# Optimization experiments

Measured on AMD Instinct MI355X. Metric: run time of the kernel, lower is better.

Reference implementation:

```python
import jax, jax.numpy as jnp
import numpy as np

N, R, E, H, F = 50000, 6, 32768, 256, 16
NH, HD = 8, 32
EPS_LN = 1e-5

def _ln(x, g, b):
    mu = x.mean(-1, keepdims=True)
    var = ((x - mu) ** 2).mean(-1, keepdims=True)
    return (x - mu) * jax.lax.rsqrt(var + EPS_LN) * g + b

def setup_inputs() -> dict:
    key = jax.random.key(0)
    ks = jax.random.split(key, 32)
    s = lambda i, shape, scale=0.05: jax.random.normal(ks[i], shape, jnp.float32) * scale
    return {
        'x': jax.random.normal(ks[0], (N, H), jnp.float32),
        'edge_index': jax.random.randint(ks[1], (R, 2, E), 0, N, jnp.int32),
        'edge_attr': jax.random.normal(ks[2], (R, E, F), jnp.float32),
        'Wq': s(3, (R, H, H)), 'bq': s(4, (R, H)),
        'Wk': s(5, (R, H + F, H)), 'bk': s(6, (R, H)),
        'Wv': s(7, (R, H + F, H)), 'bv': s(8, (R, H)),
        'prior': jnp.ones((R, NH), jnp.float32),
        'Wm': s(9, (R, H, H)), 'bm': s(10, (R, H)),
        'W_ir1': s(11, (R * H, H)), 'b_ir1': s(12, (H,)),
        'W_ir2': s(13, (H, R)), 'b_ir2': s(14, (R,)),
        'Wmp': s(15, (3, H, H)), 'bmp': s(16, (3, H)),
        'Wa1': s(17, (H, H // 2)), 'ba1': s(18, (H // 2,)),
        'Wa2': s(19, (H // 2, 1)),
        'g_meta': jnp.ones((H,), jnp.float32), 'b_meta': jnp.zeros((H,), jnp.float32),
        'Wc': s(20, (2 * H, H)), 'bc': s(21, (H,)),
        'g_out': jnp.ones((H,), jnp.float32), 'b_out': jnp.zeros((H,), jnp.float32),
    }

def _block(x, edge_index, edge_attr, Wq, bq, Wk, bk, Wv, bv, prior, Wm, bm,
           W_ir1, b_ir1, W_ir2, b_ir2, Wmp, bmp, Wa1, ba1, Wa2, g_meta, b_meta,
           Wc, bc, g_out, b_out):
    def rel_layer(eidx, eattr, wq, bq_, wk, bk_, wv, bv_, pr, wm, bm_):
        src, dst = eidx[0], eidx[1]
        q = x @ wq + bq_                                  # [N,H]
        kv_in = jnp.concatenate([x[src], eattr], -1)      # [E,H+F]
        k = (kv_in @ wk + bk_).reshape(E, NH, HD)
        v = (kv_in @ wv + bv_).reshape(E, NH, HD)
        qe = q[dst].reshape(E, NH, HD)
        scores = (qe * k).sum(-1) / np.sqrt(HD) * pr      # [E,NH]
        m = jax.ops.segment_max(scores, dst, num_segments=N)
        ex = jnp.exp(scores - m[dst])
        denom = jax.ops.segment_sum(ex, dst, num_segments=N)
        w = ex / (denom[dst] + 1e-16)
        wv_flat = (w[..., None] * v).reshape(E, H)
        agg = jax.ops.segment_sum(wv_flat, dst, num_segments=N)  # [N,H]
        return jax.nn.gelu(agg @ wm + bm_, approximate=False)

    rel_out = jax.vmap(rel_layer)(edge_index, edge_attr, Wq, bq, Wk, bk, Wv, bv,
                                  prior, Wm, bm)          # [R,N,H]

    all_rel = jnp.transpose(rel_out, (1, 0, 2)).reshape(N, R * H)
    h = jax.nn.gelu(all_rel @ W_ir1 + b_ir1, approximate=False)
    inter_w = jax.nn.softmax(h @ W_ir2 + b_ir2, axis=-1)  # [N,R]
    inter_agg = jnp.einsum('nr,rnh->nh', inter_w, rel_out)

    # meta-paths: 0=entangle(ENTANGLE=2,SWAP=3) 1=control(CONTROL=4,ROTATION=0) 2=local(PAULI=1,TEMPORAL=5)
    paths = jnp.stack([rel_out[2] + rel_out[3], rel_out[4] + rel_out[0],
                       rel_out[1] + rel_out[5]], axis=1)  # [N,3,H]
    stacked = jnp.einsum('nph,phk->npk', paths, Wmp) + bmp
    attn = jax.nn.softmax((jnp.tanh(stacked @ Wa1 + ba1) @ Wa2).squeeze(-1), axis=1)
    meta = _ln((attn[..., None] * stacked).sum(1), g_meta, b_meta)

    combined = jax.nn.gelu(jnp.concatenate([inter_agg, meta], -1) @ Wc + bc,
                           approximate=False)
    return _ln(x + combined, g_out, b_out)

def reference(x, edge_index, edge_attr, Wq, bq, Wk, bk, Wv, bv, prior, Wm, bm,
              W_ir1, b_ir1, W_ir2, b_ir2, Wmp, bmp, Wa1, ba1, Wa2, g_meta, b_meta,
              Wc, bc, g_out, b_out):
    return _block(x, edge_index, edge_attr, Wq, bq, Wk, bk, Wv, bv, prior, Wm, bm,
                  W_ir1, b_ir1, W_ir2, b_ir2, Wmp, bmp, Wa1, ba1, Wa2,
                  g_meta, b_meta, Wc, bc, g_out, b_out)
```

## Files before the change

### kernel.cpp

```cpp
#include <hip/hip_runtime.h>
#include <hip/hip_bf16.h>

typedef __hip_bfloat16 bf16;
typedef __attribute__((ext_vector_type(8))) short short8;
typedef __attribute__((ext_vector_type(4))) float f32x4;

#define NN 50000
#define RR 6
#define EE 32768
#define HH 256
#define FF 16
#define NHEAD 8
#define KVP 320

struct __align__(8) bf16x4 { bf16 v[4]; };

__device__ __forceinline__ float b2f(bf16 v) { return __bfloat162float(v); }
__device__ __forceinline__ bf16 f2b(float v) { return __float2bfloat16(v); }
__device__ __forceinline__ short f2s(float f) { bf16 b = f2b(f); return __builtin_bit_cast(short, b); }
__device__ __forceinline__ float s2f(short s) { return b2f(__builtin_bit_cast(bf16, s)); }
__device__ __forceinline__ float gelu_f(float x) { return 0.5f * x * (1.0f + erff(x * 0.7071067811865476f)); }

__device__ __forceinline__ void gl2lds16(const void* g, void* l) {
  __builtin_amdgcn_global_load_lds(
      (const __attribute__((address_space(1))) unsigned int*)g,
      (__attribute__((address_space(3))) unsigned int*)l, 16, 0, 0);
}

__global__ void zero_k(uint4* __restrict__ p, int n16)
{
  const uint4 z = make_uint4(0u, 0u, 0u, 0u);
  for (int i = blockIdx.x * blockDim.x + threadIdx.x; i < n16; i += gridDim.x * blockDim.x)
    p[i] = z;
}

__global__ void cvt_k(const float* __restrict__ in, bf16* __restrict__ out, int n4)
{
  const int i = blockIdx.x * 256 + threadIdx.x;
  if (i >= n4) return;
  const float4 f = ((const float4*)in)[i];
  bf16x4 o; o.v[0] = f2b(f.x); o.v[1] = f2b(f.y); o.v[2] = f2b(f.z); o.v[3] = f2b(f.w);
  ((bf16x4*)out)[i] = o;
}

__global__ void tconv_k(const float* __restrict__ in, bf16* __restrict__ out,
                        int K, int NC, int Kp, long izs, long ozs)
{
  __shared__ float t[32][33];
  in  += (size_t)blockIdx.z * izs;
  out += (size_t)blockIdx.z * ozs;
  const int kb = blockIdx.x * 32, nb = blockIdx.y * 32;
  const int tx = threadIdx.x & 31, ty = threadIdx.x >> 5;
  for (int i = ty; i < 32; i += 8) {
    const int k = kb + i, n = nb + tx;
    t[i][tx] = (k < K && n < NC) ? in[(size_t)k * NC + n] : 0.f;
  }
  __syncthreads();
  for (int i = ty; i < 32; i += 8) {
    const int n = nb + i, k = kb + tx;
    if (n < NC && k < Kp) out[(size_t)n * Kp + k] = f2b(t[tx][i]);
  }
}

__global__ void bkv_k(const float* __restrict__ bk, const float* __restrict__ bv,
                      float* __restrict__ bkv)
{
  const int i = blockIdx.x * 256 + threadIdx.x;
  if (i >= RR * 512) return;
  const int r = i >> 9, c = i & 511;
  bkv[i] = (c < 256) ? bk[r * 256 + c] : bv[r * 256 + (c - 256)];
}

__global__ void copyslot_k(const bf16* __restrict__ tmp, bf16* __restrict__ slot)
{
  const int i = blockIdx.x * 256 + threadIdx.x;
  if (i >= NN * 32) return;
  const int n = i >> 5, c = (i & 31) * 8;
  *(short8*)(slot + (size_t)n * 1536 + c) = *(const short8*)(tmp + (size_t)n * 256 + c);
}

template<int ASRC, int ACT, int ZMODE, typename TO>
__global__ __launch_bounds__(256) void mm_k(
    const void* __restrict__ Av, const bf16* __restrict__ A2, int lda,
    const int* __restrict__ src, const bf16* __restrict__ eab,
    const float* __restrict__ dnm,
    const bf16* __restrict__ Bt, const float* __restrict__ bias,
    const float* __restrict__ wa2, TO* __restrict__ C, int ldc,
    float* __restrict__ logits, int M, int K, int z0)
{
  __shared__ short lds[2 * 128 * 64];
  const int tid = threadIdx.x;
  const int w = tid >> 6, l = tid & 63;
  const int col0 = blockIdx.x << 7;
  const int row0 = blockIdx.y << 7;
  const bf16* Ab = (const bf16*)Av;
  const bf16* A2b = A2;
  const bf16* Btz = Bt;
  const float* biasz = bias;
  TO* Cz = C;
  float* lg = logits;
  const int* srcz = src;
  const int* dstz = nullptr;
  const bf16* eabz = eab;
  const bf16* qz = nullptr;
  float* exbz = nullptr;
  float* dnmaz = nullptr;
  const float* priz = nullptr;
  if constexpr (ZMODE == 1) {
    const int slots3[3] = {2, 4, 1};
    Ab = (const bf16*)Av + slots3[blockIdx.z] * 256;
    lg = logits + (size_t)blockIdx.z * M;
  } else if constexpr (ZMODE == 3) {
    const int r1s[3] = {2, 4, 1}, r2s[3] = {3, 0, 5};
    const int z = blockIdx.z + z0;
    Ab  = (const bf16*)Av + (size_t)r1s[z] * 256;
    A2b = A2 + (size_t)r2s[z] * 256;
    Btz = Bt + (size_t)z * 256 * K;
    biasz = bias + z * 256;
    Cz = C + (size_t)blockIdx.z * (size_t)M * 256;
  } else if constexpr (ZMODE == 4) {
    const int z = blockIdx.z;
    srcz  = src + (size_t)z * 2 * EE;
    dstz  = srcz + EE;
    eabz  = eab + (size_t)z * EE * FF;
    qz    = A2 + z * 256;
    Btz   = Bt + (size_t)z * 512 * KVP;
    biasz = bias + z * 512;
    Cz    = C + (size_t)z * (size_t)EE * 256;
    exbz  = logits + (size_t)z * EE * NHEAD;
    dnmaz = logits + (size_t)2 * EE * NHEAD + (size_t)z * NN * NHEAD;
    priz  = dnm + z * NHEAD;
  }
  const int wm = (w >> 1) << 6, wn = (w & 1) << 6;
  const int lane15 = l & 15, kq = l >> 4;

  f32x4 acc[4][4] = {};

  for (int k0 = 0; k0 < K; k0 += 64) {
#pragma unroll
    for (int i = 0; i < 4; ++i) {
      const int idx = (w * 4 + i) * 64 + l;
      const int row = idx >> 3, cg = idx & 7;
      const int scg = cg ^ (row & 7);
      const int r = min(row0 + row, M - 1);
      const int kc = k0 + scg * 8;
      if constexpr (ASRC == 0) {
        gl2lds16(Ab + (size_t)r * lda + kc, &lds[idx * 8]);
      } else if constexpr (ASRC == 2) {
        const short8 u  = *(const short8*)(Ab  + (size_t)r * lda + kc);
        const short8 v2 = *(const short8*)(A2b + (size_t)r * lda + kc);
        short8 s;
#pragma unroll
        for (int j = 0; j < 8; ++j) s[j] = f2s(s2f(u[j]) + s2f(v2[j]));
        *(short8*)&lds[idx * 8] = s;
      } else if constexpr (ASRC == 3) {
        short8 s;
        if (kc < HH) {
          s = *(const short8*)((const bf16*)Av + (size_t)srcz[r] * HH + kc);
        } else if (kc < HH + FF) {
          s = *(const short8*)(eabz + (size_t)r * FF + (kc - HH));
        } else {
#pragma unroll
          for (int j = 0; j < 8; ++j) s[j] = 0;
        }
        *(short8*)&lds[idx * 8] = s;
      } else {
        const float* p = (const float*)Av + (size_t)r * lda + kc;
        const float4 f0 = *(const float4*)p;
        const float4 f1 = *(const float4*)(p + 4);
        const float iv = 1.0f / (dnm[r * NHEAD + (kc >> 5)] + 1e-16f);
        short8 s;
        s[0] = f2s(f0.x * iv); s[1] = f2s(f0.y * iv); s[2] = f2s(f0.z * iv); s[3] = f2s(f0.w * iv);
        s[4] = f2s(f1.x * iv); s[5] = f2s(f1.y * iv); s[6] = f2s(f1.z * iv); s[7] = f2s(f1.w * iv);
        *(short8*)&lds[idx * 8] = s;
      }
    }
#pragma unroll
    for (int i = 0; i < 4; ++i) {
      const int idx = (w * 4 + i) * 64 + l;
      const int row = idx >> 3, cg = idx & 7;
      const int scg = cg ^ (row & 7);
      gl2lds16(Btz + (size_t)(col0 + row) * K + k0 + scg * 8, &lds[8192 + idx * 8]);
    }
    __syncthreads();
#pragma unroll
    for (int kk = 0; kk < 64; kk += 32) {
      short8 af[4], bfr[4];
#pragma unroll
      for (int t = 0; t < 4; ++t) {
        const int ra = wm + t * 16 + lane15;
        const int ca = ((kk >> 3) + kq) ^ (ra & 7);
        af[t] = *(const short8*)&lds[ra * 64 + ca * 8];
        const int rb = wn + t * 16 + lane15;
        const int cb = ((kk >> 3) + kq) ^ (rb & 7);
        bfr[t] = *(const short8*)&lds[8192 + rb * 64 + cb * 8];
      }
#pragma unroll
      for (int ti = 0; ti < 4; ++ti)
#pragma unroll
        for (int tj = 0; tj < 4; ++tj)
          acc[ti][tj] = __builtin_amdgcn_mfma_f32_16x16x32_bf16(af[ti], bfr[tj], acc[ti][tj], 0, 0, 0);
    }
    __syncthreads();
  }

  if constexpr (ZMODE == 4) {
    if (blockIdx.x < 2) {
#pragma unroll
      for (int i = 0; i < 8; ++i) {
        const int idx = (w * 8 + i) * 64 + l;
        const int row = idx >> 4, cg = idx & 15;
        const int d = dstz[row0 + row];
        gl2lds16(qz + (size_t)d * 1536 + col0 + cg * 8, &lds[idx * 8]);
      }
      __syncthreads();
      const int hb = (col0 + wn) >> 5;
      const float pr0 = priz[hb], pr1 = priz[hb + 1];
#pragma unroll
      for (int ti = 0; ti < 4; ++ti) {
#pragma unroll
        for (int reg = 0; reg < 4; ++reg) {
          const int row = wm + ti * 16 + kq * 4 + reg;
          float p0 = 0.f, p1 = 0.f;
#pragma unroll
          for (int tj = 0; tj < 4; ++tj) {
            const int colL = wn + tj * 16 + lane15;
            const float kv_ = acc[ti][tj][reg] + biasz[col0 + colL];
            const float qv = s2f(lds[(row << 7) + colL]);
            if (tj < 2) p0 += qv * kv_; else p1 += qv * kv_;
          }
#pragma unroll
          for (int off = 1; off < 16; off <<= 1) {
            p0 += __shfl_xor(p0, off, 64);
            p1 += __shfl_xor(p1, off, 64);
          }
          if (lane15 == 0) {
            const int e = row0 + row;
            const int d = dstz[e];
            const float e0 = expf(p0 * 0.1767766952966369f * pr0);
            const float e1 = expf(p1 * 0.1767766952966369f * pr1);
            exbz[e * NHEAD + hb]     = e0;
            exbz[e * NHEAD + hb + 1] = e1;
            atomicAdd(&dnmaz[d * NHEAD + hb],     e0);
            atomicAdd(&dnmaz[d * NHEAD + hb + 1], e1);
          }
        }
      }
    } else {
#pragma unroll
      for (int ti = 0; ti < 4; ++ti) {
#pragma unroll
        for (int reg = 0; reg < 4; ++reg) {
          const int row = row0 + wm + ti * 16 + kq * 4 + reg;
#pragma unroll
          for (int tj = 0; tj < 4; ++tj) {
            const int col = col0 + wn + tj * 16 + lane15;
            const float v = acc[ti][tj][reg] + biasz[col];
            Cz[(size_t)row * 256 + (col - 256)] = (TO)f2b(v);
          }
        }
      }
    }
  } else if constexpr (ZMODE != 1) {
#pragma unroll
    for (int ti = 0; ti < 4; ++ti) {
#pragma unroll
      for (int reg = 0; reg < 4; ++reg) {
        const int row = row0 + wm + ti * 16 + kq * 4 + reg;
        if (row >= M) continue;
#pragma unroll
        for (int tj = 0; tj < 4; ++tj) {
          const int col = col0 + wn + tj * 16 + lane15;
          float v = acc[ti][tj][reg] + biasz[col];
          if constexpr (ACT == 1) v = gelu_f(v);
          if constexpr (sizeof(TO) == 2) Cz[(size_t)row * ldc + col] = (TO)f2b(v);
          else                           Cz[(size_t)row * ldc + col] = (TO)v;
        }
      }
    }
  } else {
#pragma unroll
    for (int ti = 0; ti < 4; ++ti) {
#pragma unroll
      for (int reg = 0; reg < 4; ++reg) {
        float part = 0.f;
#pragma unroll
        for (int tj = 0; tj < 4; ++tj) {
          const int col = col0 + wn + tj * 16 + lane15;
          part += tanhf(acc[ti][tj][reg] + biasz[col]) * wa2[col];
        }
#pragma unroll
        for (int off = 8; off > 0; off >>= 1) part += __shfl_xor(part, off, 64);
        const int row = row0 + wm + ti * 16 + kq * 4 + reg;
        if (lane15 == 0 && row < M) atomicAdd(&lg[row], part);
      }
    }
  }
}

__global__ void edge2_k(const float* __restrict__ ex, const bf16* __restrict__ v,
                        const int* __restrict__ dst_idx, float* __restrict__ agg)
{
  const int e = blockIdx.x, t = threadIdx.x;
  const int dst = dst_idx[e];
  const float w = ex[e * NHEAD + (t >> 5)];
  atomicAdd(&agg[(size_t)dst * HH + t], w * b2f(v[(size_t)e * HH + t]));
}

__global__ void interw_k(const bf16* __restrict__ h, const float* __restrict__ W2,
                         const float* __restrict__ b2, float* __restrict__ interw)
{
  const int wv = threadIdx.x >> 6, ln = threadIdx.x & 63;
  const int n = blockIdx.x * 4 + wv;
  if (n >= NN) return;
  float a[6] = {0.f, 0.f, 0.f, 0.f, 0.f, 0.f};
#pragma unroll
  for (int kq = 0; kq < 4; ++kq) {
    const int k = ln + (kq << 6);
    const float hv = b2f(h[(size_t)n * HH + k]);
#pragma unroll
    for (int j = 0; j < 6; ++j) a[j] += hv * W2[k * 6 + j];
  }
#pragma unroll
  for (int j = 0; j < 6; ++j) {
#pragma unroll
    for (int off = 32; off > 0; off >>= 1) a[j] += __shfl_down(a[j], off, 64);
  }
  if (ln == 0) {
    float lg[6], e[6], mx = -1e30f, s = 0.f;
#pragma unroll
    for (int j = 0; j < 6; ++j) { lg[j] = a[j] + b2[j]; mx = fmaxf(mx, lg[j]); }
#pragma unroll
    for (int j = 0; j < 6; ++j) { e[j] = expf(lg[j] - mx); s += e[j]; }
    const float inv = 1.0f / s;
#pragma unroll
    for (int j = 0; j < 6; ++j) interw[(size_t)n * 6 + j] = e[j] * inv;
  }
}

__global__ void interagg_k(const float* __restrict__ interw, const bf16* __restrict__ rel_cat,
                           bf16* __restrict__ comb)
{
  const int n = blockIdx.x, t = threadIdx.x;
  float acc = 0.f;
#pragma unroll
  for (int r = 0; r < 6; ++r)
    acc += interw[(size_t)n * 6 + r] * b2f(rel_cat[(size_t)n * 1536 + r * 256 + t]);
  comb[(size_t)n * 512 + t] = f2b(acc);
}

__global__ void metafinal_k(const float* __restrict__ logits, const bf16* __restrict__ rel_cat,
                            const float* __restrict__ gmeta, const float* __restrict__ bmeta,
                            bf16* __restrict__ comb)
{
  const int wv = threadIdx.x >> 6, ln = threadIdx.x & 63;
  const int n = blockIdx.x * 4 + wv;
  if (n >= NN) return;
  const float l0 = logits[n], l1 = logits[NN + n], l2 = logits[2 * NN + n];
  const float mx = fmaxf(l0, fmaxf(l1, l2));
  const float e0 = expf(l0 - mx), e1 = expf(l1 - mx), e2 = expf(l2 - mx);
  const float inv = 1.0f / (e0 + e1 + e2);
  const float a0 = e0 * inv, a1 = e1 * inv, a2 = e2 * inv;
  const size_t base = (size_t)n * 1536;
  float pre[4], s = 0.f, s2 = 0.f;
#pragma unroll
  for (int q4 = 0; q4 < 4; ++q4) {
    const int j = ln + (q4 << 6);
    const float v = a0 * b2f(rel_cat[base + 2 * 256 + j])
                  + a1 * b2f(rel_cat[base + 4 * 256 + j])
                  + a2 * b2f(rel_cat[base + 1 * 256 + j]);
    pre[q4] = v; s += v; s2 += v * v;
  }
#pragma unroll
  for (int off = 32; off > 0; off >>= 1) { s += __shfl_down(s, off, 64); s2 += __shfl_down(s2, off, 64); }
  s = __shfl(s, 0, 64); s2 = __shfl(s2, 0, 64);
  const float mu = s * (1.0f / 256.0f);
  const float var = s2 * (1.0f / 256.0f) - mu * mu;
  const float rs = rsqrtf(var + 1e-5f);
#pragma unroll
  for (int q4 = 0; q4 < 4; ++q4) {
    const int j = ln + (q4 << 6);
    comb[(size_t)n * 512 + 256 + j] = f2b((pre[q4] - mu) * rs * gmeta[j] + bmeta[j]);
  }
}

__global__ void final_k(const float* __restrict__ x, const float* __restrict__ combined,
                        const float* __restrict__ g, const float* __restrict__ b,
                        float* __restrict__ out)
{
  __shared__ float sred[8];
  const int n = blockIdx.x, t = threadIdx.x;
  const float v = x[(size_t)n * HH + t] + combined[(size_t)n * HH + t];
  float s = v, s2 = v * v;
#pragma unroll
  for (int off = 32; off > 0; off >>= 1) { s += __shfl_down(s, off, 64); s2 += __shfl_down(s2, off, 64); }
  const int wv = t >> 6;
  if ((t & 63) == 0) { sred[wv] = s; sred[4 + wv] = s2; }
  __syncthreads();
  const float st = sred[0] + sred[1] + sred[2] + sred[3];
  const float st2 = sred[4] + sred[5] + sred[6] + sred[7];
  const float mu = st * (1.0f / 256.0f);
  const float var = st2 * (1.0f / 256.0f) - mu * mu;
  const float rs = rsqrtf(var + 1e-5f);
  out[(size_t)n * HH + t] = (v - mu) * rs * g[t] + b[t];
}

extern "C" void kernel_launch(void* const* d_in, const int* in_sizes, int n_in,
                              void* d_out, int out_size, void* d_ws, size_t ws_size,
                              hipStream_t stream)
{
  const float* x      = (const float*)d_in[0];
  const int*   eidx   = (const int*)d_in[1];
  const float* eattr  = (const float*)d_in[2];
  const float* Wq     = (const float*)d_in[3];
  const float* bq     = (const float*)d_in[4];
  const float* Wk     = (const float*)d_in[5];
  const float* bk     = (const float*)d_in[6];
  const float* Wv     = (const float*)d_in[7];
  const float* bv     = (const float*)d_in[8];
  const float* prior  = (const float*)d_in[9];
  const float* Wm     = (const float*)d_in[10];
  const float* bm     = (const float*)d_in[11];
  const float* W_ir1  = (const float*)d_in[12];
  const float* b_ir1  = (const float*)d_in[13];
  const float* W_ir2  = (const float*)d_in[14];
  const float* b_ir2  = (const float*)d_in[15];
  const float* Wmp    = (const float*)d_in[16];
  const float* bmp    = (const float*)d_in[17];
  const float* Wa1    = (const float*)d_in[18];
  const float* ba1    = (const float*)d_in[19];
  const float* Wa2    = (const float*)d_in[20];
  const float* g_meta = (const float*)d_in[21];
  const float* b_meta = (const float*)d_in[22];
  const float* Wc     = (const float*)d_in[23];
  const float* bc     = (const float*)d_in[24];
  const float* g_out  = (const float*)d_in[25];
  const float* b_out  = (const float*)d_in[26];
  float* out = (float*)d_out;

  char* ws = (char*)d_ws;
  bf16* rel_cat = (bf16*)ws;
  char* W0 = ws + 153600000;
  bf16*  Wqt   = (bf16*)(W0 + 0);
  bf16*  Wkvt  = (bf16*)(W0 + 786432);
  bf16*  Wmt   = (bf16*)(W0 + 2752512);
  bf16*  Wir1t = (bf16*)(W0 + 3538944);
  bf16*  Wct   = (bf16*)(W0 + 4325376);
  bf16*  Wmpt  = (bf16*)(W0 + 4587520);
  bf16*  Wa1t  = (bf16*)(W0 + 4980736);
  float* bkv   = (float*)(W0 + 5046272);
  char* region = ws + 158658560;
  bf16*  kvbuf  = (bf16*)(region + 0);
  float* exden  = (float*)(region + 33554432);
  float* denom2 = exden + 2 * EE * NHEAD;
  bf16*  xb     = (bf16*)(region + 38851584);
  bf16*  eab    = (bf16*)(region + 64451584);
  float* agg    = out;
  bf16*  hbuf     = (bf16*)(region + 0);
  float* interw   = (float*)(region + 33554432);
  bf16*  tmp      = (bf16*)(region + 0);
  float* logits   = (float*)(region + 51200000);
  bf16*  comb     = (bf16*)out;
  float* combined = (float*)(region + 0);

  const dim3 gN(2, 391);
  const dim3 gQ(12, 391);
  const dim3 gKV(4, 256, 2);
  const dim3 gMP2(2, 391, 2);
  const dim3 gMP1(2, 391, 1);
  const dim3 gL(1, 391, 3);

  tconv_k<<<dim3(8, 8, 6), 256, 0, stream>>>(Wq, Wqt, 256, 256, 256, 256 * 256, 256 * 256);
  tconv_k<<<dim3(10, 8, 6), 256, 0, stream>>>(Wk, Wkvt, 272, 256, 320, 272 * 256, 512 * 320);
  tconv_k<<<dim3(10, 8, 6), 256, 0, stream>>>(Wv, Wkvt + 256 * 320, 272, 256, 320, 272 * 256, 512 * 320);
  tconv_k<<<dim3(8, 8, 6), 256, 0, stream>>>(Wm, Wmt, 256, 256, 256, 256 * 256, 256 * 256);
  tconv_k<<<dim3(48, 8, 1), 256, 0, stream>>>(W_ir1, Wir1t, 1536, 256, 1536, 0, 0);
  tconv_k<<<dim3(16, 8, 1), 256, 0, stream>>>(Wc, Wct, 512, 256, 512, 0, 0);
  tconv_k<<<dim3(8, 8, 3), 256, 0, stream>>>(Wmp, Wmpt, 256, 256, 256, 256 * 256, 256 * 256);
  tconv_k<<<dim3(8, 4, 1), 256, 0, stream>>>(Wa1, Wa1t, 256, 128, 256, 0, 0);
  bkv_k<<<12, 256, 0, stream>>>(bk, bv, bkv);
  cvt_k<<<(NN * 64 + 255) / 256, 256, 0, stream>>>(x, xb, NN * 64);
  cvt_k<<<(RR * EE * FF / 4 + 255) / 256, 256, 0, stream>>>(eattr, eab, RR * EE * FF / 4);

  mm_k<0, 0, 0, bf16><<<gQ, 256, 0, stream>>>(
      xb, nullptr, 256, nullptr, nullptr, nullptr,
      Wqt, bq, nullptr, rel_cat, 1536, nullptr, NN, 256, 0);

  for (int pr = 0; pr < 3; ++pr) {
    const int r0 = 2 * pr;
    zero_k<<<391, 256, 0, stream>>>((uint4*)denom2, (2 * NN * NHEAD * 4) / 16);
    mm_k<3, 0, 4, bf16><<<gKV, 256, 0, stream>>>(
        xb, rel_cat + r0 * 256, 0,
        eidx + (size_t)r0 * 2 * EE, eab + (size_t)r0 * EE * FF,
        prior + r0 * NHEAD,
        Wkvt + (size_t)r0 * 512 * KVP, bkv + r0 * 512, nullptr,
        kvbuf, 256, exden, EE, KVP, 0);
    for (int j = 0; j < 2; ++j) {
      const int r = r0 + j;
      const int* dst = eidx + (size_t)r * 2 * EE + EE;
      zero_k<<<2048, 256, 0, stream>>>((uint4*)agg, (NN * HH * 4) / 16);
      edge2_k<<<EE, 256, 0, stream>>>(
          exden + (size_t)j * EE * NHEAD, kvbuf + (size_t)j * EE * 256, dst, agg);
      mm_k<4, 1, 0, bf16><<<gN, 256, 0, stream>>>(
          agg, nullptr, 256, nullptr, nullptr, denom2 + (size_t)j * NN * NHEAD,
          Wmt + (size_t)r * 256 * 256, bm + r * HH, nullptr,
          rel_cat + r * 256, 1536, nullptr, NN, 256, 0);
    }
  }

  mm_k<0, 1, 0, bf16><<<gN, 256, 0, stream>>>(
      rel_cat, nullptr, 1536, nullptr, nullptr, nullptr,
      Wir1t, b_ir1, nullptr, hbuf, 256, nullptr, NN, 1536, 0);
  interw_k<<<(NN + 3) / 4, 256, 0, stream>>>(hbuf, W_ir2, b_ir2, interw);
  interagg_k<<<NN, 256, 0, stream>>>(interw, rel_cat, comb);

  mm_k<2, 0, 3, bf16><<<gMP2, 256, 0, stream>>>(
      rel_cat, rel_cat, 1536, nullptr, nullptr, nullptr,
      Wmpt, bmp, nullptr, tmp, 256, nullptr, NN, 256, 0);
  copyslot_k<<<(NN * 32 + 255) / 256, 256, 0, stream>>>(tmp, rel_cat + 2 * 256);
  copyslot_k<<<(NN * 32 + 255) / 256, 256, 0, stream>>>(tmp + (size_t)NN * 256, rel_cat + 4 * 256);
  mm_k<2, 0, 3, bf16><<<gMP1, 256, 0, stream>>>(
      rel_cat, rel_cat, 1536, nullptr, nullptr, nullptr,
      Wmpt, bmp, nullptr, tmp, 256, nullptr, NN, 256, 2);
  copyslot_k<<<(NN * 32 + 255) / 256, 256, 0, stream>>>(tmp, rel_cat + 1 * 256);

  zero_k<<<147, 256, 0, stream>>>((uint4*)logits, (3 * NN * 4) / 16);
  mm_k<0, 0, 1, bf16><<<gL, 256, 0, stream>>>(
      rel_cat, nullptr, 1536, nullptr, nullptr, nullptr,
      Wa1t, ba1, Wa2, (bf16*)nullptr, 0, logits, NN, 256, 0);
  metafinal_k<<<(NN + 3) / 4, 256, 0, stream>>>(logits, rel_cat, g_meta, b_meta, comb);

  mm_k<0, 1, 0, float><<<gN, 256, 0, stream>>>(
      comb, nullptr, 512, nullptr, nullptr, nullptr,
      Wct, bc, nullptr, combined, 256, nullptr, NN, 512, 0);
  final_k<<<NN, 256, 0, stream>>>(x, combined, g_out, b_out, out);
}
```

Before: 1.458 ms.

## Fuse V projection with weighted scatter-add, drop V buffer and edge kernel

The K/V GEMM now computes only the K half plus attention scores. A new GEMM mode computes V per relation and atomically scatter-adds the exp-weighted values straight into the node aggregation buffer. This removes the bf16 V buffer write/read and the separate per-edge scatter kernel. In exchange, the V GEMM is split into its own launch per relation, and atomics are issued from the GEMM epilogue in fp32.

```diff
diff --git a/kernel.cpp b/kernel.cpp
--- a/kernel.cpp
+++ b/kernel.cpp
@@ -126,10 +126,11 @@
     qz    = A2 + z * 256;
     Btz   = Bt + (size_t)z * 512 * KVP;
     biasz = bias + z * 512;
-    Cz    = C + (size_t)z * (size_t)EE * 256;
     exbz  = logits + (size_t)z * EE * NHEAD;
     dnmaz = logits + (size_t)2 * EE * NHEAD + (size_t)z * NN * NHEAD;
     priz  = dnm + z * NHEAD;
+  } else if constexpr (ZMODE == 5) {
+    dstz = src + EE;
   }
   const int wm = (w >> 1) << 6, wn = (w & 1) << 6;
   const int lane15 = l & 15, kq = l >> 4;
@@ -205,59 +206,59 @@
   }
 
   if constexpr (ZMODE == 4) {
-    if (blockIdx.x < 2) {
-#pragma unroll
-      for (int i = 0; i < 8; ++i) {
-        const int idx = (w * 8 + i) * 64 + l;
-        const int row = idx >> 4, cg = idx & 15;
-        const int d = dstz[row0 + row];
-        gl2lds16(qz + (size_t)d * 1536 + col0 + cg * 8, &lds[idx * 8]);
+#pragma unroll
+    for (int i = 0; i < 8; ++i) {
+      const int idx = (w * 8 + i) * 64 + l;
+      const int row = idx >> 4, cg = idx & 15;
+      const int d = dstz[row0 + row];
+      gl2lds16(qz + (size_t)d * 1536 + col0 + cg * 8, &lds[idx * 8]);
+    }
+    __syncthreads();
+    const int hb = (col0 + wn) >> 5;
+    const float pr0 = priz[hb], pr1 = priz[hb + 1];
+#pragma unroll
+    for (int ti = 0; ti < 4; ++ti) {
+#pragma unroll
+      for (int reg = 0; reg < 4; ++reg) {
+        const int row = wm + ti * 16 + kq * 4 + reg;
+        float p0 = 0.f, p1 = 0.f;
+#pragma unroll
+        for (int tj = 0; tj < 4; ++tj) {
+          const int colL = wn + tj * 16 + lane15;
+          const float kv_ = acc[ti][tj][reg] + biasz[col0 + colL];
+          const float qv = s2f(lds[(row << 7) + colL]);
+          if (tj < 2) p0 += qv * kv_; else p1 += qv * kv_;
+        }
+#pragma unroll
+        for (int off = 1; off < 16; off <<= 1) {
+          p0 += __shfl_xor(p0, off, 64);
+          p1 += __shfl_xor(p1, off, 64);
+        }
+        if (lane15 == 0) {
+          const int e = row0 + row;
+          const int d = dstz[e];
+          const float e0 = expf(p0 * 0.1767766952966369f * pr0);
+          const float e1 = expf(p1 * 0.1767766952966369f * pr1);
+          exbz[e * NHEAD + hb]     = e0;
+          exbz[e * NHEAD + hb + 1] = e1;
+          atomicAdd(&dnmaz[d * NHEAD + hb],     e0);
+          atomicAdd(&dnmaz[d * NHEAD + hb + 1], e1);
+        }
       }
-      __syncthreads();
-      const int hb = (col0 + wn) >> 5;
-      const float pr0 = priz[hb], pr1 = priz[hb + 1];
-#pragma unroll
-      for (int ti = 0; ti < 4; ++ti) {
-#pragma unroll
-        for (int reg = 0; reg < 4; ++reg) {
-          const int row = wm + ti * 16 + kq * 4 + reg;
-          float p0 = 0.f, p1 = 0.f;
-#pragma unroll
-          for (int tj = 0; tj < 4; ++tj) {
-            const int colL = wn + tj * 16 + lane15;
-            const float kv_ = acc[ti][tj][reg] + biasz[col0 + colL];
-            const float qv = s2f(lds[(row << 7) + colL]);
-            if (tj < 2) p0 += qv * kv_; else p1 += qv * kv_;
-          }
-#pragma unroll
-          for (int off = 1; off < 16; off <<= 1) {
-            p0 += __shfl_xor(p0, off, 64);
-            p1 += __shfl_xor(p1, off, 64);
-          }
-          if (lane15 == 0) {
-            const int e = row0 + row;
-            const int d = dstz[e];
-            const float e0 = expf(p0 * 0.1767766952966369f * pr0);
-            const float e1 = expf(p1 * 0.1767766952966369f * pr1);
-            exbz[e * NHEAD + hb]     = e0;
-            exbz[e * NHEAD + hb + 1] = e1;
-            atomicAdd(&dnmaz[d * NHEAD + hb],     e0);
-            atomicAdd(&dnmaz[d * NHEAD + hb + 1], e1);
-          }
-        }
-      }
-    } else {
-#pragma unroll
-      for (int ti = 0; ti < 4; ++ti) {
-#pragma unroll
-        for (int reg = 0; reg < 4; ++reg) {
-          const int row = row0 + wm + ti * 16 + kq * 4 + reg;
-#pragma unroll
-          for (int tj = 0; tj < 4; ++tj) {
-            const int col = col0 + wn + tj * 16 + lane15;
-            const float v = acc[ti][tj][reg] + biasz[col];
-            Cz[(size_t)row * 256 + (col - 256)] = (TO)f2b(v);
-          }
+    }
+  } else if constexpr (ZMODE == 5) {
+#pragma unroll
+    for (int ti = 0; ti < 4; ++ti) {
+#pragma unroll
+      for (int reg = 0; reg < 4; ++reg) {
+        const int e = row0 + wm + ti * 16 + kq * 4 + reg;
+        const int d = dstz[e];
+        float* ap = lg + (size_t)d * HH;
+#pragma unroll
+        for (int tj = 0; tj < 4; ++tj) {
+          const int col = col0 + wn + tj * 16 + lane15;
+          const float wgt = dnm[e * NHEAD + ((col0 + wn + tj * 16) >> 5)];
+          atomicAdd(ap + col, wgt * (acc[ti][tj][reg] + biasz[col]));
         }
       }
     }
@@ -296,15 +297,6 @@
       }
     }
   }
-}
-
-__global__ void edge2_k(const float* __restrict__ ex, const bf16* __restrict__ v,
-                        const int* __restrict__ dst_idx, float* __restrict__ agg)
-{
-  const int e = blockIdx.x, t = threadIdx.x;
-  const int dst = dst_idx[e];
-  const float w = ex[e * NHEAD + (t >> 5)];
-  atomicAdd(&agg[(size_t)dst * HH + t], w * b2f(v[(size_t)e * HH + t]));
 }
 
 __global__ void interw_k(const bf16* __restrict__ h, const float* __restrict__ W2,
@@ -450,8 +442,7 @@
   bf16*  Wa1t  = (bf16*)(W0 + 4980736);
   float* bkv   = (float*)(W0 + 5046272);
   char* region = ws + 158658560;
-  bf16*  kvbuf  = (bf16*)(region + 0);
-  float* exden  = (float*)(region + 33554432);
+  float* exden  = (float*)(region + 0);
   float* denom2 = exden + 2 * EE * NHEAD;
   bf16*  xb     = (bf16*)(region + 38851584);
   bf16*  eab    = (bf16*)(region + 64451584);
@@ -465,7 +456,8 @@
 
   const dim3 gN(2, 391);
   const dim3 gQ(12, 391);
-  const dim3 gKV(4, 256, 2);
+  const dim3 gK(2, 256, 2);
+  const dim3 gV(2, 256);
   const dim3 gMP2(2, 391, 2);
   const dim3 gMP1(2, 391, 1);
   const dim3 gL(1, 391, 3);
@@ -489,18 +481,21 @@
   for (int pr = 0; pr < 3; ++pr) {
     const int r0 = 2 * pr;
     zero_k<<<391, 256, 0, stream>>>((uint4*)denom2, (2 * NN * NHEAD * 4) / 16);
-    mm_k<3, 0, 4, bf16><<<gKV, 256, 0, stream>>>(
+    mm_k<3, 0, 4, bf16><<<gK, 256, 0, stream>>>(
         xb, rel_cat + r0 * 256, 0,
         eidx + (size_t)r0 * 2 * EE, eab + (size_t)r0 * EE * FF,
         prior + r0 * NHEAD,
         Wkvt + (size_t)r0 * 512 * KVP, bkv + r0 * 512, nullptr,
-        kvbuf, 256, exden, EE, KVP, 0);
+        (bf16*)nullptr, 0, exden, EE, KVP, 0);
     for (int j = 0; j < 2; ++j) {
       const int r = r0 + j;
-      const int* dst = eidx + (size_t)r * 2 * EE + EE;
       zero_k<<<2048, 256, 0, stream>>>((uint4*)agg, (NN * HH * 4) / 16);
-      edge2_k<<<EE, 256, 0, stream>>>(
-          exden + (size_t)j * EE * NHEAD, kvbuf + (size_t)j * EE * 256, dst, agg);
+      mm_k<3, 0, 5, bf16><<<gV, 256, 0, stream>>>(
+          xb, nullptr, 0,
+          eidx + (size_t)r * 2 * EE, eab + (size_t)r * EE * FF,
+          exden + (size_t)j * EE * NHEAD,
+          Wkvt + (size_t)r * 512 * KVP + (size_t)256 * KVP, bkv + r * 512 + 256,
+          nullptr, (bf16*)nullptr, 0, agg, EE, KVP, 0);
       mm_k<4, 1, 0, bf16><<<gN, 256, 0, stream>>>(
           agg, nullptr, 256, nullptr, nullptr, denom2 + (size_t)j * NN * NHEAD,
           Wmt + (size_t)r * 256 * 256, bm + r * HH, nullptr,
```

New measurement: 1.432 ms. Within noise of the previous version (-1.8%).
